# Kernel tuning notes

Hardware: AMD Instinct MI355X
Metric: run time of the kernel (lower is better)

Reference implementation:

```python
import jax, jax.numpy as jnp
import numpy as np

C = 768
HEADS = 12

def setup_inputs() -> dict:
    key = jax.random.key(0)
    k1, k2, k3 = jax.random.split(key, 3)
    x = jax.random.normal(k1, (8, C, 32, 32), dtype=jnp.float32)
    # 1x1 convs are channel-wise linear maps; store as [out_c, in_c]
    w_qkv = jax.random.normal(k2, (3 * C, C), dtype=jnp.float32) * (C ** -0.5)
    w_proj = jax.random.normal(k3, (C, C), dtype=jnp.float32) * (C ** -0.5)
    return {"x": x, "w_qkv": w_qkv, "w_proj": w_proj}

def reference(x, w_qkv, w_proj):
    b, c, h, w = x.shape
    heads = HEADS
    dh = c // heads
    n = h * w
    scale = dh ** -0.5
    # 1x1 conv QKV: [b, 3c, h, w] -> [b, 3, heads, dh, n]
    qkv = jnp.einsum('oc,bchw->bohw', w_qkv, x).reshape(b, 3, heads, dh, n)
    q, k, v = qkv[:, 0], qkv[:, 1], qkv[:, 2]  # each [b, heads, dh, n]
    attn = jnp.einsum('bhdn,bhdm->bhnm', q, k) * scale  # [b, heads, n, n]
    attn = jax.nn.softmax(attn, axis=-1)
    out = jnp.einsum('bhnm,bhdm->bhdn', attn, v)  # [b, heads, dh, n]
    out = out.reshape(b, c, h, w)
    return jnp.einsum('oc,bchw->bohw', w_proj, out)
```

## Files before the change

### kernel.cpp

```cpp
#include <hip/hip_runtime.h>

typedef unsigned short u16;
typedef unsigned int u32;
typedef float v4f __attribute__((ext_vector_type(4)));
typedef __bf16 bf16x8 __attribute__((ext_vector_type(8)));

#define BATCH 8
#define CDIM 768
#define NHEAD 12
#define DH 64
#define NSEQ 1024
#define SCL 0.18033688011112042f

#define WAIT_VM4 0xF74
#define WAIT_VM0 0xF70

__device__ __forceinline__ u16 f2bf(float f) {
  u32 u = __builtin_bit_cast(u32, f);
  u += 0x7fffu + ((u >> 16) & 1u);
  return (u16)(u >> 16);
}

__device__ __forceinline__ v4f mfma16(bf16x8 a, bf16x8 b, v4f c) {
  return __builtin_amdgcn_mfma_f32_16x16x32_bf16(a, b, c, 0, 0, 0);
}

__device__ __forceinline__ void gload16(const u16* g, u16* l) {
  __builtin_amdgcn_global_load_lds(
      (const __attribute__((address_space(1))) void*)g,
      (__attribute__((address_space(3))) void*)l, 16, 0, 0);
}

__global__ __launch_bounds__(256) void k_prep(const float* __restrict__ x,
                                              const float* __restrict__ wq,
                                              const float* __restrict__ wp,
                                              u16* __restrict__ xT,
                                              u16* __restrict__ wqb,
                                              u16* __restrict__ wpb) {
  __shared__ u16 Ts[64][72];
  int bid = blockIdx.x;
  int t = threadIdx.x;
  if (bid < 2304) {
    bool isQ = bid < 1728;
    const float* s = isQ ? wq : wp;
    u16* d = isQ ? wqb : wpb;
    int i = (isQ ? bid : bid - 1728) * 256 + t;
    float4 v = ((const float4*)s)[i];
    u32 lo = (u32)f2bf(v.x) | ((u32)f2bf(v.y) << 16);
    u32 hi = (u32)f2bf(v.z) | ((u32)f2bf(v.w) << 16);
    ((uint2*)d)[i] = uint2{lo, hi};
    return;
  }
  int id = bid - 2304;
  int p0 = (id & 15) * 64; id >>= 4;
  int c0 = (id % 12) * 64; int b = id / 12;
  int cr = t >> 4;
  int p4 = (t & 15) * 4;
  const float* src = x + ((size_t)b * CDIM + c0) * NSEQ + p0;
#pragma unroll
  for (int i = 0; i < 4; ++i) {
    int c = cr + i * 16;
    float4 v = *(const float4*)&src[(size_t)c * NSEQ + p4];
    Ts[p4 + 0][c] = f2bf(v.x);
    Ts[p4 + 1][c] = f2bf(v.y);
    Ts[p4 + 2][c] = f2bf(v.z);
    Ts[p4 + 3][c] = f2bf(v.w);
  }
  __syncthreads();
  int p = t >> 2;
  int cq = t & 3;
  u16* dst = xT + ((size_t)b * NSEQ + p0 + p) * CDIM + c0;
#pragma unroll
  for (int j = 0; j < 2; ++j) {
    int ch = cq + j * 4;
    *(int4*)&dst[ch * 8] = *(const int4*)&Ts[p][ch * 8];
  }
}

__global__ __launch_bounds__(256) void k_gemm_qkv(const u16* __restrict__ Wb,
                                                  const u16* __restrict__ xT,
                                                  u16* __restrict__ qkT,
                                                  u16* __restrict__ vbuf) {
  int oT = blockIdx.x * 128, pT = blockIdx.y * 128, b = blockIdx.z;
  __shared__ u16 As[2][128 * 32];
  __shared__ u16 Bs[2][128 * 32];
  int t = threadIdx.x, lane = t & 63, wid = t >> 6;
  int ln = lane & 15, quad = lane >> 4;
  int wr = wid >> 1, wc = wid & 1;
  v4f acc[4][4] = {};

  int lr = lane >> 2, lc = (lane & 3) * 8;
  const u16* Ag = Wb + (size_t)(oT + wid * 16 + lr) * CDIM + lc;
  const u16* Bg = xT + ((size_t)b * NSEQ + pT + wid * 16 + lr) * CDIM + lc;
  int s0 = (wid * 16) * 32, s1 = (wid * 16 + 64) * 32;

  gload16(Ag, &As[0][s0]);
  gload16(Ag + (size_t)64 * CDIM, &As[0][s1]);
  gload16(Bg, &Bs[0][s0]);
  gload16(Bg + (size_t)64 * CDIM, &Bs[0][s1]);

#pragma unroll 2
  for (int k = 0; k < 24; ++k) {
    int cur = k & 1, nxt = cur ^ 1;
    if (k < 23) {
      int kk = (k + 1) * 32;
      gload16(Ag + kk, &As[nxt][s0]);
      gload16(Ag + (size_t)64 * CDIM + kk, &As[nxt][s1]);
      gload16(Bg + kk, &Bs[nxt][s0]);
      gload16(Bg + (size_t)64 * CDIM + kk, &Bs[nxt][s1]);
      __builtin_amdgcn_s_waitcnt(WAIT_VM4);
    } else {
      __builtin_amdgcn_s_waitcnt(WAIT_VM0);
    }
    __builtin_amdgcn_s_barrier();
    bf16x8 af[4], bfr[4];
#pragma unroll
    for (int mt = 0; mt < 4; ++mt)
      af[mt] = *(const bf16x8*)&As[cur][(wr * 64 + mt * 16 + ln) * 32 + quad * 8];
#pragma unroll
    for (int nt = 0; nt < 4; ++nt)
      bfr[nt] = *(const bf16x8*)&Bs[cur][(wc * 64 + nt * 16 + ln) * 32 + quad * 8];
#pragma unroll
    for (int mt = 0; mt < 4; ++mt)
#pragma unroll
      for (int nt = 0; nt < 4; ++nt)
        acc[mt][nt] = mfma16(af[mt], bfr[nt], acc[mt][nt]);
    __builtin_amdgcn_s_barrier();
  }

  bool isV = (oT >= 2 * CDIM);
#pragma unroll
  for (int mt = 0; mt < 4; ++mt) {
#pragma unroll
    for (int nt = 0; nt < 4; ++nt) {
      int ro = oT + wr * 64 + mt * 16 + quad * 4;
      int cp = pT + wc * 64 + nt * 16 + ln;
      if (!isV) {
        u32 lo = (u32)f2bf(acc[mt][nt][0]) | ((u32)f2bf(acc[mt][nt][1]) << 16);
        u32 hi = (u32)f2bf(acc[mt][nt][2]) | ((u32)f2bf(acc[mt][nt][3]) << 16);
        *(uint2*)&qkT[((size_t)b * NSEQ + cp) * 1536 + ro] = uint2{lo, hi};
      } else {
#pragma unroll
        for (int r = 0; r < 4; ++r)
          vbuf[((size_t)b * CDIM + (ro - 2 * CDIM + r)) * NSEQ + cp] =
              f2bf(acc[mt][nt][r]);
      }
    }
  }
}

__global__ __launch_bounds__(512) void k_attn(const u16* __restrict__ qkT,
                                              const u16* __restrict__ vbuf,
                                              u16* __restrict__ attnT) {
  int id = blockIdx.x;
  int b = id & 7;
  int j = id >> 3;
  int ntile = j & 3;
  int h = j >> 2;
  int nt0 = ntile * 256;

  int t = threadIdx.x, lane = t & 63, wid = t >> 6;
  int ln = lane & 15, quad = lane >> 4;
  int nbase = nt0 + wid * 32;

  __shared__ u16 Ks[64 * 72];
  __shared__ u16 Vs[64 * 72];
  __shared__ u16 Pa[8][32 * 72];
  u16* myP = Pa[wid];

  const u16* qbase = qkT + ((size_t)b * NSEQ + nbase) * 1536 + h * DH;
  bf16x8 aq[2][2];
#pragma unroll
  for (int mt = 0; mt < 2; ++mt)
#pragma unroll
    for (int ks = 0; ks < 2; ++ks)
      aq[mt][ks] = *(const bf16x8*)&qbase[(size_t)(mt * 16 + ln) * 1536 + ks * 32 + quad * 8];

  v4f oacc[2][4] = {};
  float lsum[2] = {0.0f, 0.0f};

  const u16* kg0 = qkT + (size_t)b * NSEQ * 1536 + CDIM + h * DH;
  const u16* vg0 = vbuf + ((size_t)b * CDIM + h * DH) * NSEQ;
  int sr = t >> 3;
  int sc = (t & 7) * 8;

  for (int m0 = 0; m0 < NSEQ; m0 += 64) {
    __syncthreads();
    *(int4*)&Ks[sr * 72 + sc] = *(const int4*)(kg0 + (size_t)(m0 + sr) * 1536 + sc);
    *(int4*)&Vs[sr * 72 + sc] = *(const int4*)(vg0 + (size_t)sr * NSEQ + m0 + sc);
    __syncthreads();

#pragma unroll
    for (int ct = 0; ct < 4; ++ct) {
      bf16x8 kf0 = *(const bf16x8*)&Ks[(ct * 16 + ln) * 72 + quad * 8];
      bf16x8 kf1 = *(const bf16x8*)&Ks[(ct * 16 + ln) * 72 + 32 + quad * 8];
#pragma unroll
      for (int mt = 0; mt < 2; ++mt) {
        v4f s = {};
        s = mfma16(kf0, aq[mt][0], s);
        s = mfma16(kf1, aq[mt][1], s);
        float p0 = __builtin_amdgcn_exp2f(s[0] * SCL);
        float p1 = __builtin_amdgcn_exp2f(s[1] * SCL);
        float p2 = __builtin_amdgcn_exp2f(s[2] * SCL);
        float p3 = __builtin_amdgcn_exp2f(s[3] * SCL);
        lsum[mt] += (p0 + p1) + (p2 + p3);
        u32 lo = (u32)f2bf(p0) | ((u32)f2bf(p1) << 16);
        u32 hi = (u32)f2bf(p2) | ((u32)f2bf(p3) << 16);
        *(uint2*)&myP[(mt * 16 + ln) * 72 + ct * 16 + quad * 4] = uint2{lo, hi};
      }
    }

    bf16x8 ap[2][2];
#pragma unroll
    for (int mt = 0; mt < 2; ++mt)
#pragma unroll
      for (int ks = 0; ks < 2; ++ks)
        ap[mt][ks] = *(const bf16x8*)&myP[(mt * 16 + ln) * 72 + ks * 32 + quad * 8];
#pragma unroll
    for (int nt = 0; nt < 4; ++nt) {
      bf16x8 vf0 = *(const bf16x8*)&Vs[(nt * 16 + ln) * 72 + quad * 8];
      bf16x8 vf1 = *(const bf16x8*)&Vs[(nt * 16 + ln) * 72 + 32 + quad * 8];
#pragma unroll
      for (int mt = 0; mt < 2; ++mt) {
        oacc[mt][nt] = mfma16(ap[mt][0], vf0, oacc[mt][nt]);
        oacc[mt][nt] = mfma16(ap[mt][1], vf1, oacc[mt][nt]);
      }
    }
  }

#pragma unroll
  for (int mt = 0; mt < 2; ++mt) {
    lsum[mt] += __shfl_xor(lsum[mt], 16);
    lsum[mt] += __shfl_xor(lsum[mt], 32);
  }

#pragma unroll
  for (int mt = 0; mt < 2; ++mt) {
#pragma unroll
    for (int r = 0; r < 4; ++r) {
      float l = __shfl(lsum[mt], quad * 4 + r, 16);
      float inv = 1.0f / l;
      int n = nbase + mt * 16 + quad * 4 + r;
      u16* dst = attnT + ((size_t)b * NSEQ + n) * CDIM + h * DH;
#pragma unroll
      for (int nt = 0; nt < 4; ++nt)
        dst[nt * 16 + ln] = f2bf(oacc[mt][nt][r] * inv);
    }
  }
}

__global__ __launch_bounds__(256) void k_gemm_proj(const u16* __restrict__ Wb,
                                                   const u16* __restrict__ aT,
                                                   float* __restrict__ out) {
  int b = blockIdx.x, oT = blockIdx.y * 128, pT = blockIdx.z * 128;
  __shared__ u16 As[128 * 32];
  __shared__ u16 Bs[128 * 32];
  int t = threadIdx.x, lane = t & 63, wid = t >> 6;
  int ln = lane & 15, quad = lane >> 4;
  int wr = wid >> 1, wc = wid & 1;
  v4f acc[4][4] = {};

  int lr = lane >> 2, lc = (lane & 3) * 8;
  const u16* Ag = Wb + (size_t)(oT + wid * 16 + lr) * CDIM + lc;
  const u16* Bg = aT + ((size_t)b * NSEQ + pT + wid * 16 + lr) * CDIM + lc;
  u16* Asl = &As[(wid * 16) * 32];
  u16* Asl2 = &As[(wid * 16 + 64) * 32];
  u16* Bsl = &Bs[(wid * 16) * 32];
  u16* Bsl2 = &Bs[(wid * 16 + 64) * 32];

  for (int kk = 0; kk < CDIM; kk += 32) {
    gload16(Ag + kk, Asl);
    gload16(Ag + (size_t)64 * CDIM + kk, Asl2);
    gload16(Bg + kk, Bsl);
    gload16(Bg + (size_t)64 * CDIM + kk, Bsl2);
    __syncthreads();
    bf16x8 af[4], bfr[4];
#pragma unroll
    for (int mt = 0; mt < 4; ++mt)
      af[mt] = *(const bf16x8*)&As[(wr * 64 + mt * 16 + ln) * 32 + quad * 8];
#pragma unroll
    for (int nt = 0; nt < 4; ++nt)
      bfr[nt] = *(const bf16x8*)&Bs[(wc * 64 + nt * 16 + ln) * 32 + quad * 8];
#pragma unroll
    for (int mt = 0; mt < 4; ++mt)
#pragma unroll
      for (int nt = 0; nt < 4; ++nt)
        acc[mt][nt] = mfma16(af[mt], bfr[nt], acc[mt][nt]);
    __syncthreads();
  }

#pragma unroll
  for (int mt = 0; mt < 4; ++mt) {
#pragma unroll
    for (int nt = 0; nt < 4; ++nt) {
      int ro = oT + wr * 64 + mt * 16 + quad * 4;
      int cp = pT + wc * 64 + nt * 16 + ln;
#pragma unroll
      for (int r = 0; r < 4; ++r)
        out[((size_t)b * CDIM + ro + r) * NSEQ + cp] = acc[mt][nt][r];
    }
  }
}

extern "C" void kernel_launch(void* const* d_in, const int* in_sizes, int n_in,
                              void* d_out, int out_size, void* d_ws, size_t ws_size,
                              hipStream_t stream) {
  const float* x = (const float*)d_in[0];
  const float* w_qkv = (const float*)d_in[1];
  const float* w_proj = (const float*)d_in[2];
  float* out = (float*)d_out;

  char* ws = (char*)d_ws;
  u16* wqkv_bf = (u16*)(ws);
  u16* wproj_bf = (u16*)(ws + 3538944);
  u16* xT = (u16*)(ws + 4718592);
  u16* vbuf = (u16*)(ws + 17301504);
  u16* qkT = (u16*)d_out;
  u16* attnT = xT;

  k_prep<<<dim3(3840), dim3(256), 0, stream>>>(x, w_qkv, w_proj, xT, wqkv_bf, wproj_bf);
  k_gemm_qkv<<<dim3(18, 8, 8), dim3(256), 0, stream>>>(wqkv_bf, xT, qkT, vbuf);
  k_attn<<<dim3(384), dim3(512), 0, stream>>>(qkT, vbuf, attnT);
  k_gemm_proj<<<dim3(8, 6, 8), dim3(256), 0, stream>>>(wproj_bf, attnT, out);
}
```

Before: 206.6 us.

## Load K/V directly into registers, fold softmax scale into Q, use MFMA row sums

```diff
diff --git a/kernel.cpp b/kernel.cpp
--- a/kernel.cpp
+++ b/kernel.cpp
@@ -19,6 +19,15 @@
   u32 u = __builtin_bit_cast(u32, f);
   u += 0x7fffu + ((u >> 16) & 1u);
   return (u16)(u >> 16);
+}
+
+__device__ __forceinline__ u16 b16(float f) {
+  return (u16)((__builtin_bit_cast(u32, f) + 0x8000u) >> 16);
+}
+__device__ __forceinline__ u32 pkbf(float hi, float lo) {
+  u32 a = __builtin_bit_cast(u32, hi) + 0x8000u;
+  u32 b = __builtin_bit_cast(u32, lo) + 0x8000u;
+  return __builtin_amdgcn_perm(a, b, 0x07060302u);
 }
 
 __device__ __forceinline__ v4f mfma16(bf16x8 a, bf16x8 b, v4f c) {
@@ -129,6 +138,7 @@
   }
 
   bool isV = (oT >= 2 * CDIM);
+  float scl = (oT < CDIM) ? SCL : 1.0f;
 #pragma unroll
   for (int mt = 0; mt < 4; ++mt) {
 #pragma unroll
@@ -136,36 +146,33 @@
       int ro = oT + wr * 64 + mt * 16 + quad * 4;
       int cp = pT + wc * 64 + nt * 16 + ln;
       if (!isV) {
-        u32 lo = (u32)f2bf(acc[mt][nt][0]) | ((u32)f2bf(acc[mt][nt][1]) << 16);
-        u32 hi = (u32)f2bf(acc[mt][nt][2]) | ((u32)f2bf(acc[mt][nt][3]) << 16);
+        u32 lo = pkbf(acc[mt][nt][1] * scl, acc[mt][nt][0] * scl);
+        u32 hi = pkbf(acc[mt][nt][3] * scl, acc[mt][nt][2] * scl);
         *(uint2*)&qkT[((size_t)b * NSEQ + cp) * 1536 + ro] = uint2{lo, hi};
       } else {
 #pragma unroll
         for (int r = 0; r < 4; ++r)
           vbuf[((size_t)b * CDIM + (ro - 2 * CDIM + r)) * NSEQ + cp] =
-              f2bf(acc[mt][nt][r]);
+              b16(acc[mt][nt][r]);
       }
     }
   }
 }
 
-__global__ __launch_bounds__(512) void k_attn(const u16* __restrict__ qkT,
+__global__ __launch_bounds__(256) void k_attn(const u16* __restrict__ qkT,
                                               const u16* __restrict__ vbuf,
                                               u16* __restrict__ attnT) {
   int id = blockIdx.x;
   int b = id & 7;
   int j = id >> 3;
-  int ntile = j & 3;
-  int h = j >> 2;
-  int nt0 = ntile * 256;
+  int h = j % 12;
+  int nt0 = (j / 12) * 128;
 
   int t = threadIdx.x, lane = t & 63, wid = t >> 6;
   int ln = lane & 15, quad = lane >> 4;
   int nbase = nt0 + wid * 32;
 
-  __shared__ u16 Ks[64 * 72];
-  __shared__ u16 Vs[64 * 72];
-  __shared__ u16 Pa[8][32 * 72];
+  __shared__ u16 Pa[4][32 * 72];
   u16* myP = Pa[wid];
 
   const u16* qbase = qkT + ((size_t)b * NSEQ + nbase) * 1536 + h * DH;
@@ -176,37 +183,42 @@
     for (int ks = 0; ks < 2; ++ks)
       aq[mt][ks] = *(const bf16x8*)&qbase[(size_t)(mt * 16 + ln) * 1536 + ks * 32 + quad * 8];
 
+  bf16x8 ones;
+#pragma unroll
+  for (int i = 0; i < 8; ++i) ones[i] = __builtin_bit_cast(__bf16, (u16)0x3F80);
+
   v4f oacc[2][4] = {};
-  float lsum[2] = {0.0f, 0.0f};
-
-  const u16* kg0 = qkT + (size_t)b * NSEQ * 1536 + CDIM + h * DH;
-  const u16* vg0 = vbuf + ((size_t)b * CDIM + h * DH) * NSEQ;
-  int sr = t >> 3;
-  int sc = (t & 7) * 8;
+  v4f lacc[2] = {};
+
+  const u16* kbase = qkT + (size_t)b * NSEQ * 1536 + CDIM + h * DH;
+  const u16* vbase = vbuf + ((size_t)b * CDIM + h * DH) * NSEQ;
 
   for (int m0 = 0; m0 < NSEQ; m0 += 64) {
-    __syncthreads();
-    *(int4*)&Ks[sr * 72 + sc] = *(const int4*)(kg0 + (size_t)(m0 + sr) * 1536 + sc);
-    *(int4*)&Vs[sr * 72 + sc] = *(const int4*)(vg0 + (size_t)sr * NSEQ + m0 + sc);
-    __syncthreads();
+    bf16x8 kf[4][2], vf[4][2];
+#pragma unroll
+    for (int ct = 0; ct < 4; ++ct)
+#pragma unroll
+      for (int ks = 0; ks < 2; ++ks)
+        kf[ct][ks] = *(const bf16x8*)&kbase[(size_t)(m0 + ct * 16 + ln) * 1536 + ks * 32 + quad * 8];
+#pragma unroll
+    for (int nt = 0; nt < 4; ++nt)
+#pragma unroll
+      for (int ks = 0; ks < 2; ++ks)
+        vf[nt][ks] = *(const bf16x8*)&vbase[(size_t)(nt * 16 + ln) * NSEQ + m0 + ks * 32 + quad * 8];
 
 #pragma unroll
     for (int ct = 0; ct < 4; ++ct) {
-      bf16x8 kf0 = *(const bf16x8*)&Ks[(ct * 16 + ln) * 72 + quad * 8];
-      bf16x8 kf1 = *(const bf16x8*)&Ks[(ct * 16 + ln) * 72 + 32 + quad * 8];
 #pragma unroll
       for (int mt = 0; mt < 2; ++mt) {
         v4f s = {};
-        s = mfma16(kf0, aq[mt][0], s);
-        s = mfma16(kf1, aq[mt][1], s);
-        float p0 = __builtin_amdgcn_exp2f(s[0] * SCL);
-        float p1 = __builtin_amdgcn_exp2f(s[1] * SCL);
-        float p2 = __builtin_amdgcn_exp2f(s[2] * SCL);
-        float p3 = __builtin_amdgcn_exp2f(s[3] * SCL);
-        lsum[mt] += (p0 + p1) + (p2 + p3);
-        u32 lo = (u32)f2bf(p0) | ((u32)f2bf(p1) << 16);
-        u32 hi = (u32)f2bf(p2) | ((u32)f2bf(p3) << 16);
-        *(uint2*)&myP[(mt * 16 + ln) * 72 + ct * 16 + quad * 4] = uint2{lo, hi};
+        s = mfma16(kf[ct][0], aq[mt][0], s);
+        s = mfma16(kf[ct][1], aq[mt][1], s);
+        float p0 = __builtin_amdgcn_exp2f(s[0]);
+        float p1 = __builtin_amdgcn_exp2f(s[1]);
+        float p2 = __builtin_amdgcn_exp2f(s[2]);
+        float p3 = __builtin_amdgcn_exp2f(s[3]);
+        *(uint2*)&myP[(mt * 16 + ln) * 72 + ct * 16 + quad * 4] =
+            uint2{pkbf(p1, p0), pkbf(p3, p2)};
       }
     }
 
@@ -217,34 +229,29 @@
       for (int ks = 0; ks < 2; ++ks)
         ap[mt][ks] = *(const bf16x8*)&myP[(mt * 16 + ln) * 72 + ks * 32 + quad * 8];
 #pragma unroll
-    for (int nt = 0; nt < 4; ++nt) {
-      bf16x8 vf0 = *(const bf16x8*)&Vs[(nt * 16 + ln) * 72 + quad * 8];
-      bf16x8 vf1 = *(const bf16x8*)&Vs[(nt * 16 + ln) * 72 + 32 + quad * 8];
+    for (int mt = 0; mt < 2; ++mt) {
+      lacc[mt] = mfma16(ap[mt][0], ones, lacc[mt]);
+      lacc[mt] = mfma16(ap[mt][1], ones, lacc[mt]);
+    }
+#pragma unroll
+    for (int nt = 0; nt < 4; ++nt)
 #pragma unroll
       for (int mt = 0; mt < 2; ++mt) {
-        oacc[mt][nt] = mfma16(ap[mt][0], vf0, oacc[mt][nt]);
-        oacc[mt][nt] = mfma16(ap[mt][1], vf1, oacc[mt][nt]);
+        oacc[mt][nt] = mfma16(ap[mt][0], vf[nt][0], oacc[mt][nt]);
+        oacc[mt][nt] = mfma16(ap[mt][1], vf[nt][1], oacc[mt][nt]);
       }
-    }
   }
 
 #pragma unroll
   for (int mt = 0; mt < 2; ++mt) {
-    lsum[mt] += __shfl_xor(lsum[mt], 16);
-    lsum[mt] += __shfl_xor(lsum[mt], 32);
-  }
-
-#pragma unroll
-  for (int mt = 0; mt < 2; ++mt) {
 #pragma unroll
     for (int r = 0; r < 4; ++r) {
-      float l = __shfl(lsum[mt], quad * 4 + r, 16);
-      float inv = 1.0f / l;
+      float inv = 1.0f / lacc[mt][r];
       int n = nbase + mt * 16 + quad * 4 + r;
       u16* dst = attnT + ((size_t)b * NSEQ + n) * CDIM + h * DH;
 #pragma unroll
       for (int nt = 0; nt < 4; ++nt)
-        dst[nt * 16 + ln] = f2bf(oacc[mt][nt][r] * inv);
+        dst[nt * 16 + ln] = b16(oacc[mt][nt][r] * inv);
     }
   }
 }
@@ -320,6 +327,6 @@
 
   k_prep<<<dim3(3840), dim3(256), 0, stream>>>(x, w_qkv, w_proj, xT, wqkv_bf, wproj_bf);
   k_gemm_qkv<<<dim3(18, 8, 8), dim3(256), 0, stream>>>(wqkv_bf, xT, qkT, vbuf);
-  k_attn<<<dim3(384), dim3(512), 0, stream>>>(qkT, vbuf, attnT);
+  k_attn<<<dim3(768), dim3(256), 0, stream>>>(qkT, vbuf, attnT);
   k_gemm_proj<<<dim3(8, 6, 8), dim3(256), 0, stream>>>(wproj_bf, attnT, out);
 }
```

Result: slower. 251.5 us (+21.7%).
